# Optimization experiments

Measured on AMD Instinct MI355X. Metric: run time of the kernel, lower is better.

The kernel has to match this reference:

```python
import jax, jax.numpy as jnp
import numpy as np

VOCAB = 540
EMBED = 128   # embedding_dim, also the LSTM 'batch' dim after the faithful .view reshape
HID = 100     # hidden_size == input_size == n_visits V (forced by the code)


def setup_inputs() -> dict:
    key = jax.random.key(0)
    ks = jax.random.split(key, 9)
    B, V, C = 256, 100, 40
    diag_x = jax.random.randint(ks[0], (B, V, C), 0, VOCAB, dtype=jnp.int64)
    mask = (jax.random.uniform(ks[1], (B, V, C)) < 0.85).astype(jnp.float32)
    s_e = 1.0 / np.sqrt(EMBED)
    s_h = 1.0 / np.sqrt(HID)
    return {
        "diag_x": diag_x,
        "mask": mask,
        "embed_table": jax.random.normal(ks[2], (VOCAB, EMBED), jnp.float32),
        "W_ih": jax.random.uniform(ks[3], (4 * HID, HID), jnp.float32, -s_h, s_h),
        "W_hh": jax.random.uniform(ks[4], (4 * HID, HID), jnp.float32, -s_h, s_h),
        "b_ih": jax.random.uniform(ks[5], (4 * HID,), jnp.float32, -s_h, s_h),
        "b_hh": jax.random.uniform(ks[6], (4 * HID,), jnp.float32, -s_h, s_h),
        "fc_w": jax.random.uniform(ks[7], (1, EMBED), jnp.float32, -s_e, s_e),
        "fc_b": jax.random.uniform(ks[8], (1,), jnp.float32, -s_e, s_e),
    }


def _forward(diag_x, mask, embed_table, W_ih, W_hh, b_ih, b_hh, fc_w, fc_b):
    B, V, C = diag_x.shape
    # masked embedding sum over codes-per-visit: [B,V,C,E] -> [B,V,E]
    emb = embed_table[diag_x] * mask[..., None]
    sum_embed = jnp.sum(emb, axis=2)
    # faithful to torch .view(B, 128, -1): a RESHAPE (not transpose) mixing V and E
    x_seq = sum_embed.reshape(B, EMBED, V)   # LSTM: time=B, batch=EMBED, feat=V(=HID)

    h0 = jnp.zeros((EMBED, HID), x_seq.dtype)
    c0 = jnp.zeros((EMBED, HID), x_seq.dtype)

    def step(carry, x_t):
        h, c = carry
        gates = x_t @ W_ih.T + b_ih + h @ W_hh.T + b_hh   # [EMBED, 4*HID]
        i, f, g, o = jnp.split(gates, 4, axis=-1)          # torch gate order i,f,g,o
        i = jax.nn.sigmoid(i); f = jax.nn.sigmoid(f)
        g = jnp.tanh(g);       o = jax.nn.sigmoid(o)
        c = f * c + i * g
        h = o * jnp.tanh(c)
        return (h, c), h

    _, hs = jax.lax.scan(step, (h0, c0), x_seq)            # [B, EMBED, HID]

    # get_last_visit: per-row max index of visits with any unmasked code (segment-max)
    has_visit = jnp.sum(mask, axis=-1) > 0                 # [B, V]
    last = jnp.max(jnp.where(has_visit, jnp.arange(V), -1), axis=1)  # [B]
    true_h = jnp.take_along_axis(hs, last[:, None, None], axis=2)[:, :, 0]  # [B, EMBED]

    out = jax.nn.sigmoid(true_h @ fc_w.T + fc_b)           # [B, 1]
    return out.reshape(-1)


def reference(diag_x, mask, embed_table, W_ih, W_hh, b_ih, b_hh, fc_w, fc_b):
    return _forward(diag_x, mask, embed_table, W_ih, W_hh, b_ih, b_hh, fc_w, fc_b)
```

## Files before the change

kernel.cpp:

```cpp
#include <hip/hip_runtime.h>
#include <math.h>

#define NB 256
#define NV 100
#define NC 40
#define NE 128
#define NH 100
#define NG 400

#define OFF_SUM   0
#define N_SUM     (NB*NV*NE)
#define OFF_PRE   (OFF_SUM + N_SUM)
#define N_PRE     (NB*NE*NG)
#define OFF_TRUH  (OFF_PRE + N_PRE)
#define N_TRUH    (NB*NE)
#define OFF_LAST  (OFF_TRUH + N_TRUH)

__global__ __launch_bounds__(128) void k_embed(
    const int* __restrict__ diag, const float* __restrict__ mask,
    const float* __restrict__ table, float* __restrict__ sumembed,
    int* __restrict__ last) {
  int bv = blockIdx.x;
  int b  = bv / NV;
  int v  = bv - b * NV;
  int e = threadIdx.x;
  const float* mrow = mask + bv * NC;
  const int*   drow = diag + bv * NC;
  float acc = 0.f;
  float msum = 0.f;
  #pragma unroll
  for (int c = 0; c < NC; ++c) {
    float m = mrow[c];
    int idx = drow[c];
    acc = fmaf(m, table[idx * NE + e], acc);
    msum += m;
  }
  sumembed[bv * NE + e] = acc;
  if (e == 0 && msum > 0.f) atomicMax(&last[b], v);
}

__global__ __launch_bounds__(256) void k_pregemm(
    const float* __restrict__ x2, const float* __restrict__ Wih,
    const float* __restrict__ bih, const float* __restrict__ bhh,
    float* __restrict__ pre) {
  __shared__ __align__(16) float As[100][132];
  __shared__ __align__(16) float Bs[100][68];
  __shared__ __align__(16) float bias_s[64];
  const int m0 = blockIdx.x * 128;
  const int n0 = blockIdx.y * 64;
  const int tid = threadIdx.x;

  for (int idx = tid; idx < 12800; idx += 256) {
    int m = idx / 100, k = idx - m * 100;
    As[k][m] = x2[(m0 + m) * 100 + k];
  }
  for (int idx = tid; idx < 6400; idx += 256) {
    int n = idx / 100, k = idx - n * 100;
    int j = n0 + n;
    Bs[k][n] = (j < NG) ? Wih[j * 100 + k] : 0.f;
  }
  if (tid < 64) {
    int j = n0 + tid;
    bias_s[tid] = (j < NG) ? (bih[j] + bhh[j]) : 0.f;
  }
  __syncthreads();

  const int tm = tid & 15, tn = tid >> 4;
  float acc[8][4] = {};
  #define PG_FMA(R, AX)                                                   \
    acc[R][0] = fmaf(AX, bb.x, acc[R][0]);                                \
    acc[R][1] = fmaf(AX, bb.y, acc[R][1]);                                \
    acc[R][2] = fmaf(AX, bb.z, acc[R][2]);                                \
    acc[R][3] = fmaf(AX, bb.w, acc[R][3]);
  #pragma unroll 2
  for (int k = 0; k < 100; ++k) {
    float4 a0 = *(const float4*)&As[k][tm * 4];
    float4 a1 = *(const float4*)&As[k][64 + tm * 4];
    float4 bb = *(const float4*)&Bs[k][tn * 4];
    PG_FMA(0, a0.x) PG_FMA(1, a0.y) PG_FMA(2, a0.z) PG_FMA(3, a0.w)
    PG_FMA(4, a1.x) PG_FMA(5, a1.y) PG_FMA(6, a1.z) PG_FMA(7, a1.w)
  }
  #undef PG_FMA

  if (n0 + tn * 4 < NG) {
    float4 bb = *(const float4*)&bias_s[tn * 4];
    #pragma unroll
    for (int r = 0; r < 8; ++r) {
      int m = m0 + ((r < 4) ? (tm * 4 + r) : (64 + tm * 4 + (r - 4)));
      float4 st;
      st.x = acc[r][0] + bb.x; st.y = acc[r][1] + bb.y;
      st.z = acc[r][2] + bb.z; st.w = acc[r][3] + bb.w;
      *(float4*)&pre[m * NG + n0 + tn * 4] = st;
    }
  }
}

__device__ __forceinline__ float fast_sigmoid(float x) {
  return 1.f / (1.f + __expf(-x));
}
__device__ __forceinline__ float fast_tanh(float x) {
  float ax = fabsf(x);
  float e  = __expf(-2.f * ax);
  float t  = (1.f - e) / (1.f + e);
  return x < 0.f ? -t : t;
}

#define FMA4(A, W, H)                                                     \
  A = fmaf((H).x, (W).x, A); A = fmaf((H).y, (W).y, A);                   \
  A = fmaf((H).z, (W).z, A); A = fmaf((H).w, (W).w, A)

__global__ __launch_bounds__(512, 2) void k_lstm(
    const float* __restrict__ pre, const float* __restrict__ Whh,
    const int* __restrict__ last, float* __restrict__ truh) {
  __shared__ __align__(16) float h_s[100];
  __shared__ float g_s[NG];
  __shared__ int   last_s[NB];
  const int e = blockIdx.x;
  const int j = threadIdx.x;

  float4 w00, w01, w02, w03, w04, w05, w06, w07, w08, w09, w10, w11, w12,
         w13, w14, w15, w16, w17, w18, w19, w20, w21, w22, w23, w24;
  if (j < NG) {
    const float4* wr = (const float4*)(Whh + j * 100);
    w00 = wr[0];  w01 = wr[1];  w02 = wr[2];  w03 = wr[3];  w04 = wr[4];
    w05 = wr[5];  w06 = wr[6];  w07 = wr[7];  w08 = wr[8];  w09 = wr[9];
    w10 = wr[10]; w11 = wr[11]; w12 = wr[12]; w13 = wr[13]; w14 = wr[14];
    w15 = wr[15]; w16 = wr[16]; w17 = wr[17]; w18 = wr[18]; w19 = wr[19];
    w20 = wr[20]; w21 = wr[21]; w22 = wr[22]; w23 = wr[23]; w24 = wr[24];
  }
  if (j < NH) h_s[j] = 0.f;
  if (j < NB) last_s[j] = last[j];
  float c = 0.f;

  const float* pbase = pre + e * NG + j;
  float p0 = (j < NG) ? pbase[0]         : 0.f;
  float p1 = (j < NG) ? pbase[51200]     : 0.f;
  float p2 = (j < NG) ? pbase[2 * 51200] : 0.f;
  __syncthreads();

  for (int t = 0; t < NB; ++t) {
    float p3 = (j < NG && t + 3 < NB) ? pbase[(t + 3) * 51200] : 0.f;

    if (j < NG) {
      float a0 = p0, a1 = 0.f, a2 = 0.f, a3 = 0.f;
      const float4* h4 = (const float4*)h_s;
      float4 h;
      h = h4[0];  FMA4(a0, w00, h);
      h = h4[1];  FMA4(a1, w01, h);
      h = h4[2];  FMA4(a2, w02, h);
      h = h4[3];  FMA4(a3, w03, h);
      h = h4[4];  FMA4(a0, w04, h);
      h = h4[5];  FMA4(a1, w05, h);
      h = h4[6];  FMA4(a2, w06, h);
      h = h4[7];  FMA4(a3, w07, h);
      h = h4[8];  FMA4(a0, w08, h);
      h = h4[9];  FMA4(a1, w09, h);
      h = h4[10]; FMA4(a2, w10, h);
      h = h4[11]; FMA4(a3, w11, h);
      h = h4[12]; FMA4(a0, w12, h);
      h = h4[13]; FMA4(a1, w13, h);
      h = h4[14]; FMA4(a2, w14, h);
      h = h4[15]; FMA4(a3, w15, h);
      h = h4[16]; FMA4(a0, w16, h);
      h = h4[17]; FMA4(a1, w17, h);
      h = h4[18]; FMA4(a2, w18, h);
      h = h4[19]; FMA4(a3, w19, h);
      h = h4[20]; FMA4(a0, w20, h);
      h = h4[21]; FMA4(a1, w21, h);
      h = h4[22]; FMA4(a2, w22, h);
      h = h4[23]; FMA4(a3, w23, h);
      h = h4[24]; FMA4(a0, w24, h);
      float acc = (a0 + a1) + (a2 + a3);
      float act = (j >= 200 && j < 300) ? fast_tanh(acc) : fast_sigmoid(acc);
      g_s[j] = act;
    }
    __syncthreads();

    if (j < NH) {
      float ig = g_s[j], fg = g_s[100 + j], gg = g_s[200 + j], og = g_s[300 + j];
      c = fmaf(fg, c, ig * gg);
      float h = og * fast_tanh(c);
      h_s[j] = h;
      if (j == last_s[t]) truh[t * NE + e] = h;
    }
    __syncthreads();

    p0 = p1; p1 = p2; p2 = p3;
  }
}

__global__ __launch_bounds__(128) void k_fc(
    const float* __restrict__ truh, const float* __restrict__ fcw,
    const float* __restrict__ fcb, float* __restrict__ out) {
  int b = blockIdx.x, t = threadIdx.x;
  float v = truh[b * NE + t] * fcw[t];
  #pragma unroll
  for (int o = 32; o > 0; o >>= 1) v += __shfl_down(v, o);
  __shared__ float s[2];
  if ((t & 63) == 0) s[t >> 6] = v;
  __syncthreads();
  if (t == 0) {
    float sum = s[0] + s[1] + fcb[0];
    out[b] = 1.f / (1.f + __expf(-sum));
  }
}

extern "C" void kernel_launch(void* const* d_in, const int* in_sizes, int n_in,
                              void* d_out, int out_size, void* d_ws, size_t ws_size,
                              hipStream_t stream) {
  (void)in_sizes; (void)n_in; (void)out_size; (void)ws_size;
  const int*   diag  = (const int*)d_in[0];
  const float* mask  = (const float*)d_in[1];
  const float* table = (const float*)d_in[2];
  const float* Wih   = (const float*)d_in[3];
  const float* Whh   = (const float*)d_in[4];
  const float* bih   = (const float*)d_in[5];
  const float* bhh   = (const float*)d_in[6];
  const float* fcw   = (const float*)d_in[7];
  const float* fcb   = (const float*)d_in[8];

  float* ws       = (float*)d_ws;
  float* sumembed = ws + OFF_SUM;
  float* pre      = ws + OFF_PRE;
  float* truh     = ws + OFF_TRUH;
  int*   last     = (int*)(ws + OFF_LAST);
  float* out      = (float*)d_out;

  hipMemsetAsync(last, 0, NB * sizeof(int), stream);
  k_embed  <<<dim3(NB * NV), dim3(128), 0, stream>>>(diag, mask, table, sumembed, last);
  k_pregemm<<<dim3(256, 7),  dim3(256), 0, stream>>>(sumembed, Wih, bih, bhh, pre);
  k_lstm   <<<dim3(NE),      dim3(512), 0, stream>>>(pre, Whh, last, truh);
  k_fc     <<<dim3(NB),      dim3(128), 0, stream>>>(truh, fcw, fcb, out);
}
```

Baseline: 439.6 us.

## Fuse embedding, input GEMM and LSTM into one producer/consumer kernel with flags

Merges the embedding-sum, input-projection GEMM and LSTM recurrence into a single persistent kernel. 128 producer blocks compute per-timestep embeddings into shared memory, run the GEMM for that timestep, and publish a per-timestep release flag that also carries the last-visit index. 128 consumer blocks run the recurrence and spin on these flags, so the serial LSTM can start while later timesteps are still being produced. This removes the sumembed round trip and two launches. It relies on all 256 blocks being co-resident to avoid deadlock, and each producer now does the whole GEMM for its timestep.

```diff
diff --git a/kernel.cpp b/kernel.cpp
--- a/kernel.cpp
+++ b/kernel.cpp
@@ -8,92 +8,11 @@
 #define NH 100
 #define NG 400
 
-#define OFF_SUM   0
-#define N_SUM     (NB*NV*NE)
-#define OFF_PRE   (OFF_SUM + N_SUM)
+#define OFF_PRE   0
 #define N_PRE     (NB*NE*NG)
 #define OFF_TRUH  (OFF_PRE + N_PRE)
 #define N_TRUH    (NB*NE)
-#define OFF_LAST  (OFF_TRUH + N_TRUH)
-
-__global__ __launch_bounds__(128) void k_embed(
-    const int* __restrict__ diag, const float* __restrict__ mask,
-    const float* __restrict__ table, float* __restrict__ sumembed,
-    int* __restrict__ last) {
-  int bv = blockIdx.x;
-  int b  = bv / NV;
-  int v  = bv - b * NV;
-  int e = threadIdx.x;
-  const float* mrow = mask + bv * NC;
-  const int*   drow = diag + bv * NC;
-  float acc = 0.f;
-  float msum = 0.f;
-  #pragma unroll
-  for (int c = 0; c < NC; ++c) {
-    float m = mrow[c];
-    int idx = drow[c];
-    acc = fmaf(m, table[idx * NE + e], acc);
-    msum += m;
-  }
-  sumembed[bv * NE + e] = acc;
-  if (e == 0 && msum > 0.f) atomicMax(&last[b], v);
-}
-
-__global__ __launch_bounds__(256) void k_pregemm(
-    const float* __restrict__ x2, const float* __restrict__ Wih,
-    const float* __restrict__ bih, const float* __restrict__ bhh,
-    float* __restrict__ pre) {
-  __shared__ __align__(16) float As[100][132];
-  __shared__ __align__(16) float Bs[100][68];
-  __shared__ __align__(16) float bias_s[64];
-  const int m0 = blockIdx.x * 128;
-  const int n0 = blockIdx.y * 64;
-  const int tid = threadIdx.x;
-
-  for (int idx = tid; idx < 12800; idx += 256) {
-    int m = idx / 100, k = idx - m * 100;
-    As[k][m] = x2[(m0 + m) * 100 + k];
-  }
-  for (int idx = tid; idx < 6400; idx += 256) {
-    int n = idx / 100, k = idx - n * 100;
-    int j = n0 + n;
-    Bs[k][n] = (j < NG) ? Wih[j * 100 + k] : 0.f;
-  }
-  if (tid < 64) {
-    int j = n0 + tid;
-    bias_s[tid] = (j < NG) ? (bih[j] + bhh[j]) : 0.f;
-  }
-  __syncthreads();
-
-  const int tm = tid & 15, tn = tid >> 4;
-  float acc[8][4] = {};
-  #define PG_FMA(R, AX)                                                   \
-    acc[R][0] = fmaf(AX, bb.x, acc[R][0]);                                \
-    acc[R][1] = fmaf(AX, bb.y, acc[R][1]);                                \
-    acc[R][2] = fmaf(AX, bb.z, acc[R][2]);                                \
-    acc[R][3] = fmaf(AX, bb.w, acc[R][3]);
-  #pragma unroll 2
-  for (int k = 0; k < 100; ++k) {
-    float4 a0 = *(const float4*)&As[k][tm * 4];
-    float4 a1 = *(const float4*)&As[k][64 + tm * 4];
-    float4 bb = *(const float4*)&Bs[k][tn * 4];
-    PG_FMA(0, a0.x) PG_FMA(1, a0.y) PG_FMA(2, a0.z) PG_FMA(3, a0.w)
-    PG_FMA(4, a1.x) PG_FMA(5, a1.y) PG_FMA(6, a1.z) PG_FMA(7, a1.w)
-  }
-  #undef PG_FMA
-
-  if (n0 + tn * 4 < NG) {
-    float4 bb = *(const float4*)&bias_s[tn * 4];
-    #pragma unroll
-    for (int r = 0; r < 8; ++r) {
-      int m = m0 + ((r < 4) ? (tm * 4 + r) : (64 + tm * 4 + (r - 4)));
-      float4 st;
-      st.x = acc[r][0] + bb.x; st.y = acc[r][1] + bb.y;
-      st.z = acc[r][2] + bb.z; st.w = acc[r][3] + bb.w;
-      *(float4*)&pre[m * NG + n0 + tn * 4] = st;
-    }
-  }
-}
+#define OFF_FLAG  (OFF_TRUH + N_TRUH)
 
 __device__ __forceinline__ float fast_sigmoid(float x) {
   return 1.f / (1.f + __expf(-x));
@@ -109,83 +28,196 @@
   A = fmaf((H).x, (W).x, A); A = fmaf((H).y, (W).y, A);                   \
   A = fmaf((H).z, (W).z, A); A = fmaf((H).w, (W).w, A)
 
-__global__ __launch_bounds__(512, 2) void k_lstm(
-    const float* __restrict__ pre, const float* __restrict__ Whh,
-    const int* __restrict__ last, float* __restrict__ truh) {
+__global__ __launch_bounds__(512, 2) void k_fused(
+    const int* __restrict__ diag, const float* __restrict__ mask,
+    const float* __restrict__ table, const float* __restrict__ Wih,
+    const float* __restrict__ bih, const float* __restrict__ bhh,
+    const float* __restrict__ Whh, float* __restrict__ pre,
+    int* __restrict__ flag, float* __restrict__ truh) {
+  __shared__ __align__(16) float As[100][132];
+  __shared__ __align__(16) float Bs[100][132];
+  __shared__ __align__(16) float bias_s[128];
+  __shared__ int lastred[4];
   __shared__ __align__(16) float h_s[100];
   __shared__ float g_s[NG];
   __shared__ int   last_s[NB];
-  const int e = blockIdx.x;
-  const int j = threadIdx.x;
-
-  float4 w00, w01, w02, w03, w04, w05, w06, w07, w08, w09, w10, w11, w12,
-         w13, w14, w15, w16, w17, w18, w19, w20, w21, w22, w23, w24;
-  if (j < NG) {
-    const float4* wr = (const float4*)(Whh + j * 100);
-    w00 = wr[0];  w01 = wr[1];  w02 = wr[2];  w03 = wr[3];  w04 = wr[4];
-    w05 = wr[5];  w06 = wr[6];  w07 = wr[7];  w08 = wr[8];  w09 = wr[9];
-    w10 = wr[10]; w11 = wr[11]; w12 = wr[12]; w13 = wr[13]; w14 = wr[14];
-    w15 = wr[15]; w16 = wr[16]; w17 = wr[17]; w18 = wr[18]; w19 = wr[19];
-    w20 = wr[20]; w21 = wr[21]; w22 = wr[22]; w23 = wr[23]; w24 = wr[24];
-  }
-  if (j < NH) h_s[j] = 0.f;
-  if (j < NB) last_s[j] = last[j];
-  float c = 0.f;
-
-  const float* pbase = pre + e * NG + j;
-  float p0 = (j < NG) ? pbase[0]         : 0.f;
-  float p1 = (j < NG) ? pbase[51200]     : 0.f;
-  float p2 = (j < NG) ? pbase[2 * 51200] : 0.f;
-  __syncthreads();
-
-  for (int t = 0; t < NB; ++t) {
-    float p3 = (j < NG && t + 3 < NB) ? pbase[(t + 3) * 51200] : 0.f;
-
+  __shared__ int   ready_s;
+
+  const int tid = threadIdx.x;
+  const int bid = blockIdx.x;
+
+  if (bid < 128) {
+    const int e   = tid & 127;
+    const int sub = tid >> 7;
+    for (int rep = 0; rep < 2; ++rep) {
+      const int t = bid + rep * 128;
+      int vmax = -1;
+      for (int i = 0; i < 25; ++i) {
+        int fl = i * 512 + tid;
+        int v  = fl >> 7;
+        const float* mrow = mask + (t * NV + v) * NC;
+        const int*   drow = diag + (t * NV + v) * NC;
+        float acc = 0.f, msum = 0.f;
+        #pragma unroll 8
+        for (int c = 0; c < NC; ++c) {
+          float mm = mrow[c];
+          int idx  = drow[c];
+          acc = fmaf(mm, table[idx * NE + e], acc);
+          msum += mm;
+        }
+        int m = fl / 100, k = fl - m * 100;
+        As[k][m] = acc;
+        if (e == 0 && msum > 0.f) vmax = max(vmax, v);
+      }
+      if (e == 0) lastred[sub] = vmax;
+      __syncthreads();
+      int flagval = 0;
+      if (tid == 0) {
+        int l = max(max(lastred[0], lastred[1]), max(lastred[2], lastred[3]));
+        flagval = l + 2;
+      }
+      const int tm = tid & 15, tn = tid >> 4;
+      for (int n0 = 0; n0 < NG; n0 += 128) {
+        for (int idx = tid; idx < 12800; idx += 512) {
+          int n = idx / 100, k = idx - n * 100;
+          int jc = n0 + n;
+          Bs[k][n] = (jc < NG) ? Wih[jc * 100 + k] : 0.f;
+        }
+        if (tid < 128) {
+          int jc = n0 + tid;
+          bias_s[tid] = (jc < NG) ? (bih[jc] + bhh[jc]) : 0.f;
+        }
+        __syncthreads();
+        float acc[8][4] = {};
+        #define PG_FMA(R, AX)                                             \
+          acc[R][0] = fmaf(AX, bb.x, acc[R][0]);                          \
+          acc[R][1] = fmaf(AX, bb.y, acc[R][1]);                          \
+          acc[R][2] = fmaf(AX, bb.z, acc[R][2]);                          \
+          acc[R][3] = fmaf(AX, bb.w, acc[R][3]);
+        #pragma unroll 2
+        for (int k = 0; k < 100; ++k) {
+          float4 a0 = *(const float4*)&As[k][tm * 4];
+          float4 a1 = *(const float4*)&As[k][64 + tm * 4];
+          float4 bb = *(const float4*)&Bs[k][tn * 4];
+          PG_FMA(0, a0.x) PG_FMA(1, a0.y) PG_FMA(2, a0.z) PG_FMA(3, a0.w)
+          PG_FMA(4, a1.x) PG_FMA(5, a1.y) PG_FMA(6, a1.z) PG_FMA(7, a1.w)
+        }
+        #undef PG_FMA
+        if (n0 + tn * 4 < NG) {
+          float4 bv4 = *(const float4*)&bias_s[tn * 4];
+          #pragma unroll
+          for (int r = 0; r < 8; ++r) {
+            int m = t * 128 + ((r < 4) ? (tm * 4 + r) : (64 + tm * 4 + (r - 4)));
+            float4 st;
+            st.x = acc[r][0] + bv4.x; st.y = acc[r][1] + bv4.y;
+            st.z = acc[r][2] + bv4.z; st.w = acc[r][3] + bv4.w;
+            *(float4*)&pre[m * NG + n0 + tn * 4] = st;
+          }
+        }
+        __syncthreads();
+      }
+      if (tid == 0) {
+        __threadfence();
+        __hip_atomic_store(&flag[t], flagval, __ATOMIC_RELEASE,
+                           __HIP_MEMORY_SCOPE_AGENT);
+      }
+    }
+  } else {
+    const int e = bid - 128;
+    const int j = tid;
+
+    float4 w00, w01, w02, w03, w04, w05, w06, w07, w08, w09, w10, w11, w12,
+           w13, w14, w15, w16, w17, w18, w19, w20, w21, w22, w23, w24;
     if (j < NG) {
-      float a0 = p0, a1 = 0.f, a2 = 0.f, a3 = 0.f;
-      const float4* h4 = (const float4*)h_s;
-      float4 h;
-      h = h4[0];  FMA4(a0, w00, h);
-      h = h4[1];  FMA4(a1, w01, h);
-      h = h4[2];  FMA4(a2, w02, h);
-      h = h4[3];  FMA4(a3, w03, h);
-      h = h4[4];  FMA4(a0, w04, h);
-      h = h4[5];  FMA4(a1, w05, h);
-      h = h4[6];  FMA4(a2, w06, h);
-      h = h4[7];  FMA4(a3, w07, h);
-      h = h4[8];  FMA4(a0, w08, h);
-      h = h4[9];  FMA4(a1, w09, h);
-      h = h4[10]; FMA4(a2, w10, h);
-      h = h4[11]; FMA4(a3, w11, h);
-      h = h4[12]; FMA4(a0, w12, h);
-      h = h4[13]; FMA4(a1, w13, h);
-      h = h4[14]; FMA4(a2, w14, h);
-      h = h4[15]; FMA4(a3, w15, h);
-      h = h4[16]; FMA4(a0, w16, h);
-      h = h4[17]; FMA4(a1, w17, h);
-      h = h4[18]; FMA4(a2, w18, h);
-      h = h4[19]; FMA4(a3, w19, h);
-      h = h4[20]; FMA4(a0, w20, h);
-      h = h4[21]; FMA4(a1, w21, h);
-      h = h4[22]; FMA4(a2, w22, h);
-      h = h4[23]; FMA4(a3, w23, h);
-      h = h4[24]; FMA4(a0, w24, h);
-      float acc = (a0 + a1) + (a2 + a3);
-      float act = (j >= 200 && j < 300) ? fast_tanh(acc) : fast_sigmoid(acc);
-      g_s[j] = act;
+      const float4* wr = (const float4*)(Whh + j * 100);
+      w00 = wr[0];  w01 = wr[1];  w02 = wr[2];  w03 = wr[3];  w04 = wr[4];
+      w05 = wr[5];  w06 = wr[6];  w07 = wr[7];  w08 = wr[8];  w09 = wr[9];
+      w10 = wr[10]; w11 = wr[11]; w12 = wr[12]; w13 = wr[13]; w14 = wr[14];
+      w15 = wr[15]; w16 = wr[16]; w17 = wr[17]; w18 = wr[18]; w19 = wr[19];
+      w20 = wr[20]; w21 = wr[21]; w22 = wr[22]; w23 = wr[23]; w24 = wr[24];
     }
+    if (j < NH) h_s[j] = 0.f;
+    if (j == 0) ready_s = 0;
+    float c = 0.f;
+    const float* pbase = pre + e * NG + j;
     __syncthreads();
 
-    if (j < NH) {
-      float ig = g_s[j], fg = g_s[100 + j], gg = g_s[200 + j], og = g_s[300 + j];
-      c = fmaf(fg, c, ig * gg);
-      float h = og * fast_tanh(c);
-      h_s[j] = h;
-      if (j == last_s[t]) truh[t * NE + e] = h;
+    int ready = 0;
+    #define ENSURE(NEED)                                                  \
+      while (ready < (NEED)) {                                            \
+        int f = 0;                                                        \
+        int fidx = ready + j;                                             \
+        if (j < 64 && fidx < NB)                                          \
+          f = __hip_atomic_load(&flag[fidx], __ATOMIC_ACQUIRE,            \
+                                __HIP_MEMORY_SCOPE_AGENT);                \
+        if (f != 0) last_s[fidx] = f - 2;                                 \
+        unsigned long long bal = __ballot(f != 0);                        \
+        if (j == 0) {                                                     \
+          int adv = (~bal == 0ULL) ? 64 : (__ffsll((long long)~bal) - 1); \
+          ready_s = ready + adv;                                          \
+        }                                                                 \
+        __syncthreads();                                                  \
+        ready = ready_s;                                                  \
+        __syncthreads();                                                  \
+      }
+
+    ENSURE(3);
+    float p0 = (j < NG) ? pbase[0]         : 0.f;
+    float p1 = (j < NG) ? pbase[51200]     : 0.f;
+    float p2 = (j < NG) ? pbase[2 * 51200] : 0.f;
+
+    for (int t = 0; t < NB; ++t) {
+      int need = (t + 4 < NB) ? (t + 4) : NB;
+      ENSURE(need);
+      float p3 = (j < NG && t + 3 < NB) ? pbase[(t + 3) * 51200] : 0.f;
+
+      if (j < NG) {
+        float a0 = p0, a1 = 0.f, a2 = 0.f, a3 = 0.f;
+        const float4* h4 = (const float4*)h_s;
+        float4 h;
+        h = h4[0];  FMA4(a0, w00, h);
+        h = h4[1];  FMA4(a1, w01, h);
+        h = h4[2];  FMA4(a2, w02, h);
+        h = h4[3];  FMA4(a3, w03, h);
+        h = h4[4];  FMA4(a0, w04, h);
+        h = h4[5];  FMA4(a1, w05, h);
+        h = h4[6];  FMA4(a2, w06, h);
+        h = h4[7];  FMA4(a3, w07, h);
+        h = h4[8];  FMA4(a0, w08, h);
+        h = h4[9];  FMA4(a1, w09, h);
+        h = h4[10]; FMA4(a2, w10, h);
+        h = h4[11]; FMA4(a3, w11, h);
+        h = h4[12]; FMA4(a0, w12, h);
+        h = h4[13]; FMA4(a1, w13, h);
+        h = h4[14]; FMA4(a2, w14, h);
+        h = h4[15]; FMA4(a3, w15, h);
+        h = h4[16]; FMA4(a0, w16, h);
+        h = h4[17]; FMA4(a1, w17, h);
+        h = h4[18]; FMA4(a2, w18, h);
+        h = h4[19]; FMA4(a3, w19, h);
+        h = h4[20]; FMA4(a0, w20, h);
+        h = h4[21]; FMA4(a1, w21, h);
+        h = h4[22]; FMA4(a2, w22, h);
+        h = h4[23]; FMA4(a3, w23, h);
+        h = h4[24]; FMA4(a0, w24, h);
+        float acc = (a0 + a1) + (a2 + a3);
+        float act = (j >= 200 && j < 300) ? fast_tanh(acc) : fast_sigmoid(acc);
+        g_s[j] = act;
+      }
+      __syncthreads();
+
+      if (j < NH) {
+        float ig = g_s[j], fg = g_s[100 + j], gg = g_s[200 + j], og = g_s[300 + j];
+        c = fmaf(fg, c, ig * gg);
+        float h = og * fast_tanh(c);
+        h_s[j] = h;
+        if (j == last_s[t]) truh[t * NE + e] = h;
+      }
+      __syncthreads();
+
+      p0 = p1; p1 = p2; p2 = p3;
     }
-    __syncthreads();
-
-    p0 = p1; p1 = p2; p2 = p3;
+    #undef ENSURE
   }
 }
 
@@ -219,16 +251,14 @@
   const float* fcw   = (const float*)d_in[7];
   const float* fcb   = (const float*)d_in[8];
 
-  float* ws       = (float*)d_ws;
-  float* sumembed = ws + OFF_SUM;
-  float* pre      = ws + OFF_PRE;
-  float* truh     = ws + OFF_TRUH;
-  int*   last     = (int*)(ws + OFF_LAST);
-  float* out      = (float*)d_out;
-
-  hipMemsetAsync(last, 0, NB * sizeof(int), stream);
-  k_embed  <<<dim3(NB * NV), dim3(128), 0, stream>>>(diag, mask, table, sumembed, last);
-  k_pregemm<<<dim3(256, 7),  dim3(256), 0, stream>>>(sumembed, Wih, bih, bhh, pre);
-  k_lstm   <<<dim3(NE),      dim3(512), 0, stream>>>(pre, Whh, last, truh);
-  k_fc     <<<dim3(NB),      dim3(128), 0, stream>>>(truh, fcw, fcb, out);
-}
+  float* ws   = (float*)d_ws;
+  float* pre  = ws + OFF_PRE;
+  float* truh = ws + OFF_TRUH;
+  int*   flag = (int*)(ws + OFF_FLAG);
+  float* out  = (float*)d_out;
+
+  hipMemsetAsync(flag, 0, NB * sizeof(int), stream);
+  k_fused<<<dim3(256), dim3(512), 0, stream>>>(
+      diag, mask, table, Wih, bih, bhh, Whh, pre, flag, truh);
+  k_fc<<<dim3(NB), dim3(128), 0, stream>>>(truh, fcw, fcb, out);
+}
```

Result: slower. 660.7 us (+50.3%).
